# Performance work log

Hardware: AMD Instinct MI355X
Metric: run time of the kernel (lower is better)

Reference implementation:

```python
import jax, jax.numpy as jnp
import numpy as np

NEAR, FAR = 2.0, 6.0
N_SAMPLE = 128  # fine samples per ray
EPS = 1e-5


def setup_inputs() -> dict:
    key = jax.random.key(0)
    k1, k2, k3, k4 = jax.random.split(key, 4)
    B, R, S = 8, 16384, 64
    rays_d = jax.random.normal(k1, (B, R, 3), dtype=jnp.float32)
    rays_o = jax.random.normal(k2, (B, R, 3), dtype=jnp.float32)
    # depth values along each ray, sorted ascending in [NEAR, FAR]
    z_vals = jnp.sort(
        NEAR + (FAR - NEAR) * jax.random.uniform(k3, (R, S), dtype=jnp.float32),
        axis=-1,
    )
    weights = jax.random.uniform(k4, (B, R, S), dtype=jnp.float32)
    return {"rays_d": rays_d, "rays_o": rays_o, "z_vals": z_vals, "weights": weights}


def _sample_pdf(bins, weights):
    # bins: (R, M), weights: (B, R, M-1) -> samples: (B, R, N_SAMPLE)
    weights = weights + EPS
    pdf = weights / jnp.sum(weights, axis=-1, keepdims=True)
    cdf = jnp.cumsum(pdf, axis=-1)                                   # (B, R, M-1)
    cdf = jnp.concatenate([jnp.zeros_like(cdf[..., :1]), cdf], -1)   # (B, R, M)
    B, R, M = cdf.shape
    # deterministic (linspace) samples -> reproducible reference
    u = jnp.broadcast_to(jnp.linspace(0.0, 1.0, N_SAMPLE, dtype=cdf.dtype), (B, R, N_SAMPLE))
    # batched right-side binary search
    inds = jax.vmap(jax.vmap(lambda c, uu: jnp.searchsorted(c, uu, side='right')))(cdf, u)
    below = jnp.maximum(inds - 1, 0)
    above = jnp.minimum(inds, M - 1)
    cdf_lo = jnp.take_along_axis(cdf, below, axis=-1)
    cdf_hi = jnp.take_along_axis(cdf, above, axis=-1)
    bins_b = jnp.broadcast_to(bins, (B, R, M))
    bin_lo = jnp.take_along_axis(bins_b, below, axis=-1)
    bin_hi = jnp.take_along_axis(bins_b, above, axis=-1)
    denom = cdf_hi - cdf_lo
    denom = jnp.where(denom < 1e-5, jnp.ones_like(denom), denom)
    t = (u - cdf_lo) / denom
    return bin_lo + t * (bin_hi - bin_lo)


def reference(rays_d, rays_o, z_vals, weights):
    S = z_vals.shape[-1]
    z_vals = z_vals.reshape(-1, S)                                  # (R, S)
    z_half = 0.5 * (z_vals[..., 1:] + z_vals[..., :-1])             # (R, S-1)
    z_samples = _sample_pdf(z_half, weights[..., 1:-1])             # (B, R, N)
    z_samples = jax.lax.stop_gradient(z_samples)
    B, R, N = z_samples.shape
    z_all = jnp.sort(
        jnp.concatenate([jnp.broadcast_to(z_vals, (B, R, S)), z_samples], -1), -1
    )                                                               # (B, R, S+N)
    pts = rays_o[..., None, :] + rays_d[..., None, :] * z_all[..., :, None]
    return pts, z_all
```

## Files before the change

### kernel.cpp

```cpp
#include <hip/hip_runtime.h>

#define R_RAYS 16384
#define S_VALS 64
#define NSAMP 128
#define Z_ALL 192
#define WEPS 1e-5f

typedef float f32x4 __attribute__((ext_vector_type(4)));

__device__ __forceinline__ float uval(int j) {
    return (j == 127) ? 1.0f : (float)j * (1.0f / 127.0f);
}

__global__ __launch_bounds__(256, 8) void ray_sampler_kernel(
    const float* __restrict__ rays_d,
    const float* __restrict__ rays_o,
    const float* __restrict__ z_vals,
    const float* __restrict__ weights,
    float* __restrict__ pts_out,
    float* __restrict__ zall_out)
{
    __shared__ __align__(16) float s_za[4][Z_ALL];

    const int wid  = threadIdx.x >> 6;
    const int lane = threadIdx.x & 63;
    const int ray  = blockIdx.x * 4 + wid;
    const int r    = ray & (R_RAYS - 1);

    float ox = rays_o[ray * 3 + 0], oy = rays_o[ray * 3 + 1], oz = rays_o[ray * 3 + 2];
    float dx = rays_d[ray * 3 + 0], dy = rays_d[ray * 3 + 1], dz = rays_d[ray * 3 + 2];

    float zv  = z_vals[r * S_VALS + lane];
    float zv1 = __shfl_down(zv, 1);
    float zv2 = __shfl_down(zv, 2);
    float zh  = 0.5f * (zv + zv1);
    float zh1 = 0.5f * (zv1 + zv2);

    float w = 0.0f;
    if (lane < 62) w = weights[(size_t)ray * S_VALS + lane + 1] + WEPS;
    float sc = w;
    #pragma unroll
    for (int off = 1; off < 64; off <<= 1) {
        float y = __shfl_up(sc, off);
        if (lane >= off) sc += y;
    }
    float total = __shfl(sc, 61);
    float scp   = __shfl_up(sc, 1);
    float clo = (lane == 0) ? 0.0f : scp / total;
    float chi = sc / total;
    float denom = chi - clo;
    float rden  = (denom < 1e-5f) ? 1.0f : 1.0f / denom;
    float bhi = (lane >= 62) ? zh : zh1;

    int js = (int)ceilf(clo * 127.0f);
    js = js < 0 ? 0 : (js > 128 ? 128 : js);
    while (js > 0 && uval(js - 1) >= clo) --js;
    while (js < 128 && uval(js) < clo) ++js;
    int jn = __shfl_down(js, 1);
    int je = (lane == 62) ? 128 : ((lane > 62) ? js : jn);

    int cnt_lt = 0;
    for (int j = js; j < je; ++j) {
        float u = uval(j);
        float t = (u - clo) * rden;
        float s = fmaf(t, bhi - zh, zh);
        int ind = (zv1 <= s) ? 1 : 0;
        cnt_lt += 1 - ind;
        s_za[wid][j + lane + 1 + ind] = s;
    }
    if (lane == 0) s_za[wid][0] = zv;
    if (lane <= 62) s_za[wid][lane + 1 + js + cnt_lt] = zv1;

    const float* za = s_za[wid];
    const size_t pbase = (size_t)ray * (Z_ALL * 3);
    const size_t zbase = (size_t)ray * Z_ALL;
    #pragma unroll
    for (int t = 0; t < 3; ++t) {
        int idx = lane + 64 * t;
        if (idx < 144) {
            int f0 = idx * 4;
            int s0 = f0 / 3;
            float z0 = za[s0];
            float z1 = za[s0 + 1];
            f32x4 v;
            #pragma unroll
            for (int i = 0; i < 4; ++i) {
                int gi = f0 + i;
                int s  = gi / 3;
                int c  = gi - s * 3;
                float z = (s == s0) ? z0 : z1;
                float o = (c == 0) ? ox : ((c == 1) ? oy : oz);
                float d = (c == 0) ? dx : ((c == 1) ? dy : dz);
                v[i] = fmaf(d, z, o);
            }
            __builtin_nontemporal_store(v, (f32x4*)(pts_out + pbase + f0));
        } else {
            int j = idx - 144;
            f32x4 v = *(const f32x4*)&za[j * 4];
            __builtin_nontemporal_store(v, (f32x4*)(zall_out + zbase + j * 4));
        }
    }
}

extern "C" void kernel_launch(void* const* d_in, const int* in_sizes, int n_in,
                              void* d_out, int out_size, void* d_ws, size_t ws_size,
                              hipStream_t stream) {
    const float* rays_d  = (const float*)d_in[0];
    const float* rays_o  = (const float*)d_in[1];
    const float* z_vals  = (const float*)d_in[2];
    const float* weights = (const float*)d_in[3];

    float* pts  = (float*)d_out;
    float* zall = pts + (size_t)8 * 16384 * 192 * 3;

    const int total_rays = 8 * 16384;
    dim3 grid(total_rays / 4), block(256);
    ray_sampler_kernel<<<grid, block, 0, stream>>>(rays_d, rays_o, z_vals,
                                                   weights, pts, zall);
}
```

Baseline: 99.70 us.

## Process sixteen rays per wave with software prefetch of next ray's inputs

Each wavefront now loops over 16 consecutive rays instead of handling one ray, and the grid shrinks to 2048 blocks. While the current ray is processed, the next ray's weights, z values, origin and direction are loaded into registers so load latency overlaps compute and stores. This cuts block launch overhead and per-ray setup. In exchange it uses more registers and gives the scheduler fewer independent waves, which could reduce latency hiding in what is largely a store-bound kernel.

```diff
diff --git a/kernel.cpp b/kernel.cpp
--- a/kernel.cpp
+++ b/kernel.cpp
@@ -1,15 +1,28 @@
 #include <hip/hip_runtime.h>
 
 #define R_RAYS 16384
-#define S_VALS 64
-#define NSAMP 128
 #define Z_ALL 192
 #define WEPS 1e-5f
+#define RPW 16
+#define NBLK 2048
 
 typedef float f32x4 __attribute__((ext_vector_type(4)));
 
 __device__ __forceinline__ float uval(int j) {
     return (j == 127) ? 1.0f : (float)j * (1.0f / 127.0f);
+}
+
+struct RayIn { float w, zv, ox, oy, oz, dx, dy, dz; };
+
+__device__ __forceinline__ void load_ray(RayIn& in,
+    const float* __restrict__ rays_d, const float* __restrict__ rays_o,
+    const float* __restrict__ z_vals, const float* __restrict__ weights,
+    int ray, int lane)
+{
+    in.w  = (lane < 62) ? weights[(size_t)ray * 64 + (lane + 1)] : 0.0f;
+    in.zv = z_vals[(ray & (R_RAYS - 1)) * 64 + lane];
+    in.ox = rays_o[ray * 3 + 0]; in.oy = rays_o[ray * 3 + 1]; in.oz = rays_o[ray * 3 + 2];
+    in.dx = rays_d[ray * 3 + 0]; in.dy = rays_d[ray * 3 + 1]; in.dz = rays_d[ray * 3 + 2];
 }
 
 __global__ __launch_bounds__(256, 8) void ray_sampler_kernel(
@@ -24,81 +37,89 @@
 
     const int wid  = threadIdx.x >> 6;
     const int lane = threadIdx.x & 63;
-    const int ray  = blockIdx.x * 4 + wid;
-    const int r    = ray & (R_RAYS - 1);
+    int ray = (blockIdx.x * 4 + wid) * RPW;
 
-    float ox = rays_o[ray * 3 + 0], oy = rays_o[ray * 3 + 1], oz = rays_o[ray * 3 + 2];
-    float dx = rays_d[ray * 3 + 0], dy = rays_d[ray * 3 + 1], dz = rays_d[ray * 3 + 2];
+    RayIn cur;
+    load_ray(cur, rays_d, rays_o, z_vals, weights, ray, lane);
 
-    float zv  = z_vals[r * S_VALS + lane];
-    float zv1 = __shfl_down(zv, 1);
-    float zv2 = __shfl_down(zv, 2);
-    float zh  = 0.5f * (zv + zv1);
-    float zh1 = 0.5f * (zv1 + zv2);
+    #pragma unroll 1
+    for (int i = 0; i < RPW; ++i) {
+        RayIn nxt = cur;
+        if (i + 1 < RPW)
+            load_ray(nxt, rays_d, rays_o, z_vals, weights, ray + 1, lane);
 
-    float w = 0.0f;
-    if (lane < 62) w = weights[(size_t)ray * S_VALS + lane + 1] + WEPS;
-    float sc = w;
-    #pragma unroll
-    for (int off = 1; off < 64; off <<= 1) {
-        float y = __shfl_up(sc, off);
-        if (lane >= off) sc += y;
-    }
-    float total = __shfl(sc, 61);
-    float scp   = __shfl_up(sc, 1);
-    float clo = (lane == 0) ? 0.0f : scp / total;
-    float chi = sc / total;
-    float denom = chi - clo;
-    float rden  = (denom < 1e-5f) ? 1.0f : 1.0f / denom;
-    float bhi = (lane >= 62) ? zh : zh1;
+        float zv  = cur.zv;
+        float zv1 = __shfl_down(zv, 1);
+        float zv2 = __shfl_down(zv, 2);
+        float zh  = 0.5f * (zv + zv1);
+        float zh1 = 0.5f * (zv1 + zv2);
 
-    int js = (int)ceilf(clo * 127.0f);
-    js = js < 0 ? 0 : (js > 128 ? 128 : js);
-    while (js > 0 && uval(js - 1) >= clo) --js;
-    while (js < 128 && uval(js) < clo) ++js;
-    int jn = __shfl_down(js, 1);
-    int je = (lane == 62) ? 128 : ((lane > 62) ? js : jn);
+        float w = (lane < 62) ? cur.w + WEPS : 0.0f;
+        float sc = w;
+        #pragma unroll
+        for (int off = 1; off < 64; off <<= 1) {
+            float y = __shfl_up(sc, off);
+            if (lane >= off) sc += y;
+        }
+        float total = __shfl(sc, 61);
+        float scp   = __shfl_up(sc, 1);
+        float clo = (lane == 0) ? 0.0f : scp / total;
+        float chi = sc / total;
+        float denom = chi - clo;
+        float rden  = (denom < 1e-5f) ? 1.0f : 1.0f / denom;
+        float bhi = (lane >= 62) ? zh : zh1;
 
-    int cnt_lt = 0;
-    for (int j = js; j < je; ++j) {
-        float u = uval(j);
-        float t = (u - clo) * rden;
-        float s = fmaf(t, bhi - zh, zh);
-        int ind = (zv1 <= s) ? 1 : 0;
-        cnt_lt += 1 - ind;
-        s_za[wid][j + lane + 1 + ind] = s;
-    }
-    if (lane == 0) s_za[wid][0] = zv;
-    if (lane <= 62) s_za[wid][lane + 1 + js + cnt_lt] = zv1;
+        int js = (int)ceilf(clo * 127.0f);
+        js = js < 0 ? 0 : (js > 128 ? 128 : js);
+        while (js > 0 && uval(js - 1) >= clo) --js;
+        while (js < 128 && uval(js) < clo) ++js;
+        int jn = __shfl_down(js, 1);
+        int je = (lane == 62) ? 128 : ((lane > 62) ? js : jn);
 
-    const float* za = s_za[wid];
-    const size_t pbase = (size_t)ray * (Z_ALL * 3);
-    const size_t zbase = (size_t)ray * Z_ALL;
-    #pragma unroll
-    for (int t = 0; t < 3; ++t) {
-        int idx = lane + 64 * t;
-        if (idx < 144) {
-            int f0 = idx * 4;
-            int s0 = f0 / 3;
-            float z0 = za[s0];
-            float z1 = za[s0 + 1];
-            f32x4 v;
-            #pragma unroll
-            for (int i = 0; i < 4; ++i) {
-                int gi = f0 + i;
-                int s  = gi / 3;
-                int c  = gi - s * 3;
-                float z = (s == s0) ? z0 : z1;
-                float o = (c == 0) ? ox : ((c == 1) ? oy : oz);
-                float d = (c == 0) ? dx : ((c == 1) ? dy : dz);
-                v[i] = fmaf(d, z, o);
+        int cnt_lt = 0;
+        for (int j = js; j < je; ++j) {
+            float u = uval(j);
+            float t = (u - clo) * rden;
+            float s = fmaf(t, bhi - zh, zh);
+            int ind = (zv1 <= s) ? 1 : 0;
+            cnt_lt += 1 - ind;
+            s_za[wid][j + lane + 1 + ind] = s;
+        }
+        if (lane == 0) s_za[wid][0] = zv;
+        if (lane <= 62) s_za[wid][lane + 1 + js + cnt_lt] = zv1;
+
+        const float* za = s_za[wid];
+        const size_t pbase = (size_t)ray * (Z_ALL * 3);
+        const size_t zbase = (size_t)ray * Z_ALL;
+        #pragma unroll
+        for (int t = 0; t < 3; ++t) {
+            int idx = lane + 64 * t;
+            if (idx < 144) {
+                int f0 = idx * 4;
+                int s0 = f0 / 3;
+                float z0 = za[s0];
+                float z1 = za[s0 + 1];
+                f32x4 v;
+                #pragma unroll
+                for (int q = 0; q < 4; ++q) {
+                    int gi = f0 + q;
+                    int s  = gi / 3;
+                    int c  = gi - s * 3;
+                    float z = (s == s0) ? z0 : z1;
+                    float o = (c == 0) ? cur.ox : ((c == 1) ? cur.oy : cur.oz);
+                    float d = (c == 0) ? cur.dx : ((c == 1) ? cur.dy : cur.dz);
+                    v[q] = fmaf(d, z, o);
+                }
+                __builtin_nontemporal_store(v, (f32x4*)(pts_out + pbase + f0));
+            } else {
+                int j = idx - 144;
+                f32x4 v = *(const f32x4*)&za[j * 4];
+                __builtin_nontemporal_store(v, (f32x4*)(zall_out + zbase + j * 4));
             }
-            __builtin_nontemporal_store(v, (f32x4*)(pts_out + pbase + f0));
-        } else {
-            int j = idx - 144;
-            f32x4 v = *(const f32x4*)&za[j * 4];
-            __builtin_nontemporal_store(v, (f32x4*)(zall_out + zbase + j * 4));
         }
+
+        cur = nxt;
+        ++ray;
     }
 }
 
@@ -113,8 +134,7 @@
     float* pts  = (float*)d_out;
     float* zall = pts + (size_t)8 * 16384 * 192 * 3;
 
-    const int total_rays = 8 * 16384;
-    dim3 grid(total_rays / 4), block(256);
+    dim3 grid(NBLK), block(256);
     ray_sampler_kernel<<<grid, block, 0, stream>>>(rays_d, rays_o, z_vals,
                                                    weights, pts, zall);
 }
```

Result: slower. 123.8 us (+24.1%).

## Split fused ray sampler into separate zall and pts kernels

Applied to the files above, without the earlier changes.

Splits the single fused kernel into two launches. One computes the sorted z_all per ray and writes it to global memory; the other reads z_all back and expands it into 3D points. This isolates the sampling/sort stage from the point-expansion stage, possibly to improve occupancy by dropping the occupancy hint. The cost is an extra round trip of the z_all array through global memory and a second kernel launch.

```diff
diff --git a/kernel.cpp b/kernel.cpp
--- a/kernel.cpp
+++ b/kernel.cpp
@@ -1,8 +1,6 @@
 #include <hip/hip_runtime.h>
 
 #define R_RAYS 16384
-#define S_VALS 64
-#define NSAMP 128
 #define Z_ALL 192
 #define WEPS 1e-5f
 
@@ -12,12 +10,9 @@
     return (j == 127) ? 1.0f : (float)j * (1.0f / 127.0f);
 }
 
-__global__ __launch_bounds__(256, 8) void ray_sampler_kernel(
-    const float* __restrict__ rays_d,
-    const float* __restrict__ rays_o,
+__global__ __launch_bounds__(256) void zall_kernel(
     const float* __restrict__ z_vals,
     const float* __restrict__ weights,
-    float* __restrict__ pts_out,
     float* __restrict__ zall_out)
 {
     __shared__ __align__(16) float s_za[4][Z_ALL];
@@ -27,17 +22,14 @@
     const int ray  = blockIdx.x * 4 + wid;
     const int r    = ray & (R_RAYS - 1);
 
-    float ox = rays_o[ray * 3 + 0], oy = rays_o[ray * 3 + 1], oz = rays_o[ray * 3 + 2];
-    float dx = rays_d[ray * 3 + 0], dy = rays_d[ray * 3 + 1], dz = rays_d[ray * 3 + 2];
-
-    float zv  = z_vals[r * S_VALS + lane];
+    float zv  = z_vals[r * 64 + lane];
     float zv1 = __shfl_down(zv, 1);
     float zv2 = __shfl_down(zv, 2);
     float zh  = 0.5f * (zv + zv1);
     float zh1 = 0.5f * (zv1 + zv2);
 
     float w = 0.0f;
-    if (lane < 62) w = weights[(size_t)ray * S_VALS + lane + 1] + WEPS;
+    if (lane < 62) w = weights[(size_t)ray * 64 + lane + 1] + WEPS;
     float sc = w;
     #pragma unroll
     for (int off = 1; off < 64; off <<= 1) {
@@ -71,9 +63,33 @@
     if (lane == 0) s_za[wid][0] = zv;
     if (lane <= 62) s_za[wid][lane + 1 + js + cnt_lt] = zv1;
 
+    if (lane < 48) {
+        f32x4 v = *(const f32x4*)&s_za[wid][lane * 4];
+        *(f32x4*)(zall_out + (size_t)ray * Z_ALL + lane * 4) = v;
+    }
+}
+
+__global__ __launch_bounds__(256) void pts_kernel(
+    const float* __restrict__ rays_d,
+    const float* __restrict__ rays_o,
+    const float* __restrict__ zall,
+    float* __restrict__ pts_out)
+{
+    __shared__ __align__(16) float s_za[4][Z_ALL];
+
+    const int wid  = threadIdx.x >> 6;
+    const int lane = threadIdx.x & 63;
+    const int ray  = blockIdx.x * 4 + wid;
+
+    if (lane < 48) {
+        f32x4 v = *(const f32x4*)(zall + (size_t)ray * Z_ALL + lane * 4);
+        *(f32x4*)&s_za[wid][lane * 4] = v;
+    }
+    float ox = rays_o[ray * 3 + 0], oy = rays_o[ray * 3 + 1], oz = rays_o[ray * 3 + 2];
+    float dx = rays_d[ray * 3 + 0], dy = rays_d[ray * 3 + 1], dz = rays_d[ray * 3 + 2];
+
     const float* za = s_za[wid];
     const size_t pbase = (size_t)ray * (Z_ALL * 3);
-    const size_t zbase = (size_t)ray * Z_ALL;
     #pragma unroll
     for (int t = 0; t < 3; ++t) {
         int idx = lane + 64 * t;
@@ -84,20 +100,16 @@
             float z1 = za[s0 + 1];
             f32x4 v;
             #pragma unroll
-            for (int i = 0; i < 4; ++i) {
-                int gi = f0 + i;
+            for (int q = 0; q < 4; ++q) {
+                int gi = f0 + q;
                 int s  = gi / 3;
                 int c  = gi - s * 3;
                 float z = (s == s0) ? z0 : z1;
                 float o = (c == 0) ? ox : ((c == 1) ? oy : oz);
                 float d = (c == 0) ? dx : ((c == 1) ? dy : dz);
-                v[i] = fmaf(d, z, o);
+                v[q] = fmaf(d, z, o);
             }
             __builtin_nontemporal_store(v, (f32x4*)(pts_out + pbase + f0));
-        } else {
-            int j = idx - 144;
-            f32x4 v = *(const f32x4*)&za[j * 4];
-            __builtin_nontemporal_store(v, (f32x4*)(zall_out + zbase + j * 4));
         }
     }
 }
@@ -115,6 +127,6 @@
 
     const int total_rays = 8 * 16384;
     dim3 grid(total_rays / 4), block(256);
-    ray_sampler_kernel<<<grid, block, 0, stream>>>(rays_d, rays_o, z_vals,
-                                                   weights, pts, zall);
+    zall_kernel<<<grid, block, 0, stream>>>(z_vals, weights, zall);
+    pts_kernel<<<grid, block, 0, stream>>>(rays_d, rays_o, zall, pts);
 }
```

After: 128.3 us. 1.29x slower.
